# Kernel optimization log

Measured on AMD Instinct MI355X. Metric: run time of the kernel, lower is better.

Reference implementation:

```python
import jax, jax.numpy as jnp
import numpy as np

B, T, J, C = 64, 243, 17, 128   # batch, frames (temporal nodes), joints, channels
K = 4                            # neighbour_num for top-k similarity adjacency
EPS_LN = 1e-5
EPS_BN = 1e-5
S_GCN2ATTN = 0.5                 # fixed (requires_grad=False) scale; dropout is identity in eval


def setup_inputs() -> dict:
    key = jax.random.key(0)
    ks = jax.random.split(key, 4)
    s = np.sqrt(2.0 / C).astype(np.float32)  # GCN weight init scale
    return {
        "x": jax.random.normal(ks[0], (B, T, J, C), jnp.float32),
        "attention_feat": jax.random.normal(ks[1], (B, T, J, C), jnp.float32),
        "ln_w": jnp.ones((C,), jnp.float32),
        "ln_b": jnp.zeros((C,), jnp.float32),
        "Uw": jax.random.normal(ks[2], (C, C), jnp.float32) * s,
        "Ub": jnp.zeros((C,), jnp.float32),
        "Vw": jax.random.normal(ks[3], (C, C), jnp.float32) * s,
        "Vb": jnp.zeros((C,), jnp.float32),
        "bn_w": jnp.ones((T,), jnp.float32),   # BatchNorm1d(num_nodes=T), eval mode
        "bn_b": jnp.zeros((T,), jnp.float32),
        "ls1": jnp.full((C,), 1e-5, jnp.float32),  # layer_scale_1
    }


def reference(x, attention_feat, ln_w, ln_b, Uw, Ub, Vw, Vb, bn_w, bn_b, ls1):
    res = x
    # norm1: LayerNorm over channel dim
    mu = jnp.mean(x, axis=-1, keepdims=True)
    var = jnp.mean(jnp.square(x - mu), axis=-1, keepdims=True)
    xn = (x - mu) * jax.lax.rsqrt(var + EPS_LN) * ln_w + ln_b

    # temporal GCN: (B, T, J, C) -> (B*J, T, C)
    y = jnp.transpose(xn, (0, 2, 1, 3)).reshape(B * J, T, C)

    # dynamic adjacency via top-k similarity
    sim = jnp.einsum('ntc,nsc->nts', y, y)                 # [B*J, T, T]
    thr = jax.lax.top_k(sim, K)[0][..., -1:]               # k-th largest per row
    adj = (sim >= thr).astype(y.dtype)

    # D^{-1/2} A D^{-1/2} (degrees detached in original)
    dinv = jax.lax.stop_gradient(jnp.sum(adj, axis=-1)) ** -0.5  # [B*J, T]
    norm_adj = dinv[:, :, None] * adj * dinv[:, None, :]

    agg = jnp.einsum('nts,nsc->ntc', norm_adj, y @ Vw.T + Vb)
    h = agg + y @ Uw.T + Ub
    # eval-mode BatchNorm1d over T channel (running_mean=0, running_var=1)
    h = h * (bn_w * jax.lax.rsqrt(jnp.asarray(1.0 + EPS_BN, h.dtype)))[None, :, None] + bn_b[None, :, None]
    z = jax.nn.relu(y + h)                                 # dim_in == dim_out residual

    gcn_out = jnp.transpose(z.reshape(B, J, T, C), (0, 2, 1, 3))  # back to [B, T, J, C]

    gx = ls1 * gcn_out                                     # layer_scale_1 (drop_path = identity)
    graph_feat = gx * S_GCN2ATTN                           # gcn2Attn dropout identity in eval
    out = gx + attention_feat + res
    return out, graph_feat
```

## Files before the change

kernel.cpp:

```cpp
#include <hip/hip_runtime.h>

#define B_ 64
#define T_ 243
#define J_ 17
#define C_ 128
#define JC (J_*C_)
#define NTOT (B_*T_*J_*C_)

#define YOFF    0
#define YVOFF   34816
#define NBROFF  69632
#define BNWOFF  70656
#define BNBOFF  71680
#define UBOFF   72704
#define LSOFF   73216
#define SMEM_BYTES 73728
#define YSTR 136

typedef float f32x4 __attribute__((ext_vector_type(4)));
typedef float f32x2 __attribute__((ext_vector_type(2)));

__device__ __forceinline__ unsigned pkf8(float a, float b, float c, float d){
  int p = __builtin_amdgcn_cvt_pk_fp8_f32(a, b, 0, false);
  p = __builtin_amdgcn_cvt_pk_fp8_f32(c, d, p, true);
  return (unsigned)p;
}

template<int CTRL>
__device__ __forceinline__ float dppadd(float v){
  int t = __builtin_amdgcn_update_dpp(0, __float_as_int(v), CTRL, 0xf, 0xf, true);
  return v + __int_as_float(t);
}
__device__ __forceinline__ float swz16(float v){
  return __int_as_float(__builtin_amdgcn_ds_swizzle(__float_as_int(v), 0x401F));
}

#define PINS(x, a0,a1,a2,a3) do { \
  float t_ = fmaxf(a0,(x)), m_ = fminf(a0,(x)); a0 = t_; \
  float t2_ = fmaxf(a1,m_); m_ = fminf(a1,m_); a1 = t2_; \
  float t3_ = fmaxf(a2,m_); m_ = fminf(a2,m_); a2 = t3_; \
  a3 = fmaxf(a3,m_); \
} while(0)
#define MM(p,q) do { float h_=fmaxf(p,q); q=fminf(p,q); p=h_; } while(0)

extern "C" __global__ void __launch_bounds__(1024, 8)
graphblock_kernel(const float* __restrict__ x, const float* __restrict__ att,
                  const float* __restrict__ lnw, const float* __restrict__ lnb,
                  const float* __restrict__ Uw, const float* __restrict__ Ubv,
                  const float* __restrict__ Vw, const float* __restrict__ Vbv,
                  const float* __restrict__ bnw, const float* __restrict__ bnb,
                  const float* __restrict__ ls1, float* __restrict__ out)
{
  extern __shared__ char smem[];
  const int tid = threadIdx.x;
  const int w = tid >> 6, l = tid & 63;
  const int lr = l & 15, lg = l >> 4;
  const int n = blockIdx.x, b = n / J_, j = n % J_;
  const long nbase = (long)b*T_*JC + (long)j*C_;
  const int cs = w & 7, rh = w >> 3;
  const int ch0 = cs*16 + lg*4;

  if (tid < 256) {
    bool v = tid < T_;
    ((float*)(smem+BNWOFF))[tid] = v ? bnw[tid]*rsqrtf(1.0f+1e-5f) : 0.f;
    ((float*)(smem+BNBOFF))[tid] = v ? bnb[tid] : 0.f;
  } else if (tid < 384) {
    int c = tid - 256;
    ((float*)(smem+UBOFF))[c] = Ubv[c];
    ((float*)(smem+LSOFF))[c] = ls1[c];
  }

  {
    const int lh = l >> 5, lc = l & 31;
    const float4 lw4 = *(const float4*)(lnw + lc*4);
    const float4 lb4 = *(const float4*)(lnb + lc*4);
    float4 p[8];
    #pragma unroll
    for (int i=0;i<8;i++){
      const int r = i*32 + w*2 + lh;
      p[i] = make_float4(0.f,0.f,0.f,0.f);
      if (r < T_) p[i] = *(const float4*)(x + nbase + (long)r*JC + lc*4);
    }
    #pragma unroll
    for (int i=0;i<8;i++){
      const int r = i*32 + w*2 + lh;
      unsigned pk = 0u;
      if (r < T_) {
        float4 v = p[i];
        float s = (v.x+v.y)+(v.z+v.w);
        float q = (v.x*v.x+v.y*v.y)+(v.z*v.z+v.w*v.w);
        s = dppadd<0xB1>(s);  q = dppadd<0xB1>(q);
        s = dppadd<0x4E>(s);  q = dppadd<0x4E>(q);
        s = dppadd<0x124>(s); q = dppadd<0x124>(q);
        s = dppadd<0x128>(s); q = dppadd<0x128>(q);
        s += swz16(s);        q += swz16(q);
        float mu = s*(1.f/128.f);
        float rs = rsqrtf(q*(1.f/128.f)-mu*mu+1e-5f);
        pk = pkf8((v.x-mu)*rs*lw4.x+lb4.x, (v.y-mu)*rs*lw4.y+lb4.y,
                  (v.z-mu)*rs*lw4.z+lb4.z, (v.w-mu)*rs*lw4.w+lb4.w);
      }
      *(unsigned*)(smem + YOFF + r*YSTR + lc*4) = pk;
    }
  }
  __syncthreads();

  {
    const int tcol = w*16 + lr;
    long bfr[4];
    #pragma unroll
    for (int kk=0;kk<4;kk++)
      bfr[kk] = *(const long*)(smem + YOFF + tcol*YSTR + kk*32 + lg*8);
    float v0=-3e38f, v1=-3e38f, v2=-3e38f, v3=-3e38f;
    #pragma unroll 4
    for (int st=0; st<16; st++){
      f32x4 acc = {0.f,0.f,0.f,0.f};
      #pragma unroll
      for (int kk=0;kk<4;kk++){
        long afr = *(const long*)(smem + YOFF + (st*16+lr)*YSTR + kk*32 + lg*8);
        acc = __builtin_amdgcn_mfma_f32_16x16x32_fp8_fp8(afr, bfr[kk], acc, 0,0,0);
      }
      #pragma unroll
      for (int reg=0;reg<4;reg++){
        const int sidx = st*16 + lg*4 + reg;
        unsigned u = (__float_as_uint(acc[reg]) & 0xffffff00u) | (unsigned)(sidx & 0xff);
        float pv = (sidx < T_) ? __uint_as_float(u) : -3e38f;
        PINS(pv, v0,v1,v2,v3);
      }
    }
    #pragma unroll
    for (int m=16;m<64;m<<=1){
      float c0=__shfl_xor(v0,m,64), c1=__shfl_xor(v1,m,64),
            c2=__shfl_xor(v2,m,64), c3=__shfl_xor(v3,m,64);
      float d0=fmaxf(v0,c3), d1=fmaxf(v1,c2), d2=fmaxf(v2,c1), d3=fmaxf(v3,c0);
      MM(d0,d1); MM(d2,d3); MM(d0,d2); MM(d1,d3); MM(d1,d2);
      v0=d0; v1=d1; v2=d2; v3=d3;
    }
    if (lg==0){
      unsigned pk = (__float_as_uint(v0) & 0xffu)
                  | ((__float_as_uint(v1) & 0xffu) << 8)
                  | ((__float_as_uint(v2) & 0xffu) << 16)
                  | ((__float_as_uint(v3) & 0xffu) << 24);
      *(unsigned*)(smem + NBROFF + tcol*4) = pk;
    }
  }

  long ufr[4], vfr[4];
  {
    const int crw = cs*16 + lr;
    #pragma unroll
    for (int kk=0;kk<4;kk++){
      const float4* pu = (const float4*)(Uw + crw*C_ + kk*32 + lg*8);
      float4 a = pu[0], c = pu[1];
      union { long v; unsigned u[2]; } r;
      r.u[0] = pkf8(a.x,a.y,a.z,a.w); r.u[1] = pkf8(c.x,c.y,c.z,c.w);
      ufr[kk] = r.v;
      const float4* pv = (const float4*)(Vw + crw*C_ + kk*32 + lg*8);
      a = pv[0]; c = pv[1];
      r.u[0] = pkf8(a.x,a.y,a.z,a.w); r.u[1] = pkf8(c.x,c.y,c.z,c.w);
      vfr[kk] = r.v;
    }
  }
  const float4 vb4 = *(const float4*)(Vbv + ch0);

  #pragma unroll 2
  for (int tt=0; tt<8; tt++){
    const int t = (rh*8+tt)*16 + lr;
    f32x4 accV = {0.f,0.f,0.f,0.f};
    #pragma unroll
    for (int kk=0;kk<4;kk++){
      long yf = *(const long*)(smem + YOFF + t*YSTR + kk*32 + lg*8);
      accV = __builtin_amdgcn_mfma_f32_16x16x32_fp8_fp8(vfr[kk], yf, accV, 0,0,0);
    }
    *(unsigned*)(smem + YVOFF + t*YSTR + ch0) =
        pkf8(0.25f*(accV[0]+vb4.x), 0.25f*(accV[1]+vb4.y),
             0.25f*(accV[2]+vb4.z), 0.25f*(accV[3]+vb4.w));
  }
  __syncthreads();

  const float4 ub4 = *(const float4*)((const float*)(smem+UBOFF) + ch0);
  const float4 ls4 = *(const float4*)((const float*)(smem+LSOFF) + ch0);

  int   t_n  = (rh*8)*16 + lr;
  bool  ok_n = t_n < T_;
  long  g_n  = nbase + (long)t_n*JC + ch0;
  float4 px = make_float4(0,0,0,0), pa = make_float4(0,0,0,0);
  if (ok_n){ px = *(const float4*)(x+g_n); pa = *(const float4*)(att+g_n); }

  #pragma unroll
  for (int tt=0; tt<8; tt++){
    const int   t  = t_n;
    const bool  ok = ok_n;
    const long  g  = g_n;
    const float4 x4 = px, a4 = pa;
    if (tt < 7){
      t_n  = (rh*8+tt+1)*16 + lr;
      ok_n = t_n < T_;
      g_n  = nbase + (long)t_n*JC + ch0;
      px = make_float4(0,0,0,0); pa = make_float4(0,0,0,0);
      if (ok_n){ px = *(const float4*)(x+g_n); pa = *(const float4*)(att+g_n); }
    }
    f32x4 accU = {0.f,0.f,0.f,0.f};
    #pragma unroll
    for (int kk=0;kk<4;kk++){
      long yf = *(const long*)(smem + YOFF + t*YSTR + kk*32 + lg*8);
      accU = __builtin_amdgcn_mfma_f32_16x16x32_fp8_fp8(ufr[kk], yf, accU, 0,0,0);
    }
    unsigned nb = *(const unsigned*)(smem + NBROFF + t*4);
    const int s0 = (int)(nb & 0xffu), s1 = (int)((nb>>8)&0xffu),
              s2 = (int)((nb>>16)&0xffu), s3 = (int)((nb>>24)&0xffu);
    float ag0=0,ag1=0,ag2=0,ag3=0;
    {
      unsigned q; f32x2 e, o2;
      q = *(const unsigned*)(smem+YVOFF + s0*YSTR + ch0);
      e = __builtin_amdgcn_cvt_pk_f32_fp8(q,false); o2 = __builtin_amdgcn_cvt_pk_f32_fp8(q,true);
      ag0+=e[0]; ag1+=e[1]; ag2+=o2[0]; ag3+=o2[1];
      q = *(const unsigned*)(smem+YVOFF + s1*YSTR + ch0);
      e = __builtin_amdgcn_cvt_pk_f32_fp8(q,false); o2 = __builtin_amdgcn_cvt_pk_f32_fp8(q,true);
      ag0+=e[0]; ag1+=e[1]; ag2+=o2[0]; ag3+=o2[1];
      q = *(const unsigned*)(smem+YVOFF + s2*YSTR + ch0);
      e = __builtin_amdgcn_cvt_pk_f32_fp8(q,false); o2 = __builtin_amdgcn_cvt_pk_f32_fp8(q,true);
      ag0+=e[0]; ag1+=e[1]; ag2+=o2[0]; ag3+=o2[1];
      q = *(const unsigned*)(smem+YVOFF + s3*YSTR + ch0);
      e = __builtin_amdgcn_cvt_pk_f32_fp8(q,false); o2 = __builtin_amdgcn_cvt_pk_f32_fp8(q,true);
      ag0+=e[0]; ag1+=e[1]; ag2+=o2[0]; ag3+=o2[1];
    }
    float yo0,yo1,yo2,yo3;
    {
      unsigned q = *(const unsigned*)(smem + YOFF + t*YSTR + ch0);
      f32x2 e = __builtin_amdgcn_cvt_pk_f32_fp8(q,false);
      f32x2 o2 = __builtin_amdgcn_cvt_pk_f32_fp8(q,true);
      yo0=e[0]; yo1=e[1]; yo2=o2[0]; yo3=o2[1];
    }
    const float bw = ((const float*)(smem+BNWOFF))[t];
    const float bb = ((const float*)(smem+BNBOFF))[t];
    f32x4 o, gf;
    {
      float h = (accU[0] + ag0 + ub4.x)*bw + bb;
      float gx = ls4.x * fmaxf(0.f, yo0 + h);
      o[0] = gx + a4.x + x4.x; gf[0] = gx*0.5f;
    }{
      float h = (accU[1] + ag1 + ub4.y)*bw + bb;
      float gx = ls4.y * fmaxf(0.f, yo1 + h);
      o[1] = gx + a4.y + x4.y; gf[1] = gx*0.5f;
    }{
      float h = (accU[2] + ag2 + ub4.z)*bw + bb;
      float gx = ls4.z * fmaxf(0.f, yo2 + h);
      o[2] = gx + a4.z + x4.z; gf[2] = gx*0.5f;
    }{
      float h = (accU[3] + ag3 + ub4.w)*bw + bb;
      float gx = ls4.w * fmaxf(0.f, yo3 + h);
      o[3] = gx + a4.w + x4.w; gf[3] = gx*0.5f;
    }
    if (ok){
      *(f32x4*)(out+g)      = o;
      *(f32x4*)(out+NTOT+g) = gf;
    }
  }
}

extern "C" void kernel_launch(void* const* d_in, const int* in_sizes, int n_in,
                              void* d_out, int out_size, void* d_ws, size_t ws_size,
                              hipStream_t stream) {
  hipFuncSetAttribute(reinterpret_cast<const void*>(graphblock_kernel),
                      hipFuncAttributeMaxDynamicSharedMemorySize, SMEM_BYTES);
  dim3 grid(B_ * J_);
  dim3 block(1024);
  graphblock_kernel<<<grid, block, SMEM_BYTES, stream>>>(
      (const float*)d_in[0],
      (const float*)d_in[1],
      (const float*)d_in[2],
      (const float*)d_in[3],
      (const float*)d_in[4],
      (const float*)d_in[5],
      (const float*)d_in[6],
      (const float*)d_in[7],
      (const float*)d_in[8],
      (const float*)d_in[9],
      (const float*)d_in[10],
      (float*)d_out);
}
```

Measured before the change: 194.7 us.

## Use persistent 1024-block grid with second pass for leftover graph nodes

Launches 1024 blocks instead of 1088, so the first 64 blocks each process two (b,j) graph nodes in a loop, separated by a barrier. The LayerNorm load phase is split into two halves of four rows to reduce live registers, and the V-projection loop is fully unrolled. This is meant to avoid a partial second wave of blocks, but those 64 blocks now run twice as long, which can create a tail of the same length.

Result: slower. 380.0 us (+95.2%).

```diff
diff --git a/kernel.cpp b/kernel.cpp
--- a/kernel.cpp
+++ b/kernel.cpp
@@ -6,6 +6,7 @@
 #define C_ 128
 #define JC (J_*C_)
 #define NTOT (B_*T_*J_*C_)
+#define NBLK 1088
 
 #define YOFF    0
 #define YVOFF   34816
@@ -55,8 +56,6 @@
   const int tid = threadIdx.x;
   const int w = tid >> 6, l = tid & 63;
   const int lr = l & 15, lg = l >> 4;
-  const int n = blockIdx.x, b = n / J_, j = n % J_;
-  const long nbase = (long)b*T_*JC + (long)j*C_;
   const int cs = w & 7, rh = w >> 3;
   const int ch0 = cs*16 + lg*4;
 
@@ -70,191 +69,205 @@
     ((float*)(smem+LSOFF))[c] = ls1[c];
   }
 
-  {
-    const int lh = l >> 5, lc = l & 31;
-    const float4 lw4 = *(const float4*)(lnw + lc*4);
-    const float4 lb4 = *(const float4*)(lnb + lc*4);
-    float4 p[8];
+  const int k = blockIdx.x;
+  const int niter = (k < (NBLK - 1024)) ? 2 : 1;
+
+  for (int it = 0; it < niter; ++it) {
+    const int n = k + it*1024;
+    const int b = n / J_, j = n % J_;
+    const long nbase = (long)b*T_*JC + (long)j*C_;
+
+    {
+      const int lh = l >> 5, lc = l & 31;
+      const float4 lw4 = *(const float4*)(lnw + lc*4);
+      const float4 lb4 = *(const float4*)(lnb + lc*4);
+      #pragma unroll
+      for (int half=0; half<2; half++){
+        float4 p[4];
+        #pragma unroll
+        for (int q2=0;q2<4;q2++){
+          const int r = (half*4+q2)*32 + w*2 + lh;
+          p[q2] = make_float4(0.f,0.f,0.f,0.f);
+          if (r < T_) p[q2] = *(const float4*)(x + nbase + (long)r*JC + lc*4);
+        }
+        #pragma unroll
+        for (int q2=0;q2<4;q2++){
+          const int r = (half*4+q2)*32 + w*2 + lh;
+          unsigned pk = 0u;
+          if (r < T_) {
+            float4 v = p[q2];
+            float s = (v.x+v.y)+(v.z+v.w);
+            float q = (v.x*v.x+v.y*v.y)+(v.z*v.z+v.w*v.w);
+            s = dppadd<0xB1>(s);  q = dppadd<0xB1>(q);
+            s = dppadd<0x4E>(s);  q = dppadd<0x4E>(q);
+            s = dppadd<0x124>(s); q = dppadd<0x124>(q);
+            s = dppadd<0x128>(s); q = dppadd<0x128>(q);
+            s += swz16(s);        q += swz16(q);
+            float mu = s*(1.f/128.f);
+            float rs = rsqrtf(q*(1.f/128.f)-mu*mu+1e-5f);
+            pk = pkf8((v.x-mu)*rs*lw4.x+lb4.x, (v.y-mu)*rs*lw4.y+lb4.y,
+                      (v.z-mu)*rs*lw4.z+lb4.z, (v.w-mu)*rs*lw4.w+lb4.w);
+          }
+          *(unsigned*)(smem + YOFF + r*YSTR + lc*4) = pk;
+        }
+      }
+    }
+    __syncthreads();
+
+    {
+      const int tcol = w*16 + lr;
+      long bfr[4];
+      #pragma unroll
+      for (int kk=0;kk<4;kk++)
+        bfr[kk] = *(const long*)(smem + YOFF + tcol*YSTR + kk*32 + lg*8);
+      float v0=-3e38f, v1=-3e38f, v2=-3e38f, v3=-3e38f;
+      #pragma unroll 4
+      for (int st=0; st<16; st++){
+        f32x4 acc = {0.f,0.f,0.f,0.f};
+        #pragma unroll
+        for (int kk=0;kk<4;kk++){
+          long afr = *(const long*)(smem + YOFF + (st*16+lr)*YSTR + kk*32 + lg*8);
+          acc = __builtin_amdgcn_mfma_f32_16x16x32_fp8_fp8(afr, bfr[kk], acc, 0,0,0);
+        }
+        #pragma unroll
+        for (int reg=0;reg<4;reg++){
+          const int sidx = st*16 + lg*4 + reg;
+          unsigned uu = (__float_as_uint(acc[reg]) & 0xffffff00u) | (unsigned)(sidx & 0xff);
+          float pv = (sidx < T_) ? __uint_as_float(uu) : -3e38f;
+          PINS(pv, v0,v1,v2,v3);
+        }
+      }
+      #pragma unroll
+      for (int m=16;m<64;m<<=1){
+        float c0=__shfl_xor(v0,m,64), c1=__shfl_xor(v1,m,64),
+              c2=__shfl_xor(v2,m,64), c3=__shfl_xor(v3,m,64);
+        float d0=fmaxf(v0,c3), d1=fmaxf(v1,c2), d2=fmaxf(v2,c1), d3=fmaxf(v3,c0);
+        MM(d0,d1); MM(d2,d3); MM(d0,d2); MM(d1,d3); MM(d1,d2);
+        v0=d0; v1=d1; v2=d2; v3=d3;
+      }
+      if (lg==0){
+        unsigned pk = (__float_as_uint(v0) & 0xffu)
+                    | ((__float_as_uint(v1) & 0xffu) << 8)
+                    | ((__float_as_uint(v2) & 0xffu) << 16)
+                    | ((__float_as_uint(v3) & 0xffu) << 24);
+        *(unsigned*)(smem + NBROFF + tcol*4) = pk;
+      }
+    }
+
+    long ufr[4], vfr[4];
+    {
+      const int crw = cs*16 + lr;
+      #pragma unroll
+      for (int kk=0;kk<4;kk++){
+        const float4* pu = (const float4*)(Uw + crw*C_ + kk*32 + lg*8);
+        float4 a = pu[0], c = pu[1];
+        union { long v; unsigned u[2]; } r;
+        r.u[0] = pkf8(a.x,a.y,a.z,a.w); r.u[1] = pkf8(c.x,c.y,c.z,c.w);
+        ufr[kk] = r.v;
+        const float4* pv = (const float4*)(Vw + crw*C_ + kk*32 + lg*8);
+        a = pv[0]; c = pv[1];
+        r.u[0] = pkf8(a.x,a.y,a.z,a.w); r.u[1] = pkf8(c.x,c.y,c.z,c.w);
+        vfr[kk] = r.v;
+      }
+    }
+    const float4 vb4 = *(const float4*)(Vbv + ch0);
+
+    int   t_n  = (rh*8)*16 + lr;
+    bool  ok_n = t_n < T_;
+    long  g_n  = nbase + (long)t_n*JC + ch0;
+    float4 px = make_float4(0,0,0,0), pa = make_float4(0,0,0,0);
+    if (ok_n){ px = *(const float4*)(x+g_n); pa = *(const float4*)(att+g_n); }
+
     #pragma unroll
-    for (int i=0;i<8;i++){
-      const int r = i*32 + w*2 + lh;
-      p[i] = make_float4(0.f,0.f,0.f,0.f);
-      if (r < T_) p[i] = *(const float4*)(x + nbase + (long)r*JC + lc*4);
-    }
+    for (int tt=0; tt<8; tt++){
+      const int t = (rh*8+tt)*16 + lr;
+      f32x4 accV = {0.f,0.f,0.f,0.f};
+      #pragma unroll
+      for (int kk=0;kk<4;kk++){
+        long yf = *(const long*)(smem + YOFF + t*YSTR + kk*32 + lg*8);
+        accV = __builtin_amdgcn_mfma_f32_16x16x32_fp8_fp8(vfr[kk], yf, accV, 0,0,0);
+      }
+      *(unsigned*)(smem + YVOFF + t*YSTR + ch0) =
+          pkf8(0.25f*(accV[0]+vb4.x), 0.25f*(accV[1]+vb4.y),
+               0.25f*(accV[2]+vb4.z), 0.25f*(accV[3]+vb4.w));
+    }
+    __syncthreads();
+
+    const float4 ub4 = *(const float4*)((const float*)(smem+UBOFF) + ch0);
+    const float4 ls4 = *(const float4*)((const float*)(smem+LSOFF) + ch0);
+
     #pragma unroll
-    for (int i=0;i<8;i++){
-      const int r = i*32 + w*2 + lh;
-      unsigned pk = 0u;
-      if (r < T_) {
-        float4 v = p[i];
-        float s = (v.x+v.y)+(v.z+v.w);
-        float q = (v.x*v.x+v.y*v.y)+(v.z*v.z+v.w*v.w);
-        s = dppadd<0xB1>(s);  q = dppadd<0xB1>(q);
-        s = dppadd<0x4E>(s);  q = dppadd<0x4E>(q);
-        s = dppadd<0x124>(s); q = dppadd<0x124>(q);
-        s = dppadd<0x128>(s); q = dppadd<0x128>(q);
-        s += swz16(s);        q += swz16(q);
-        float mu = s*(1.f/128.f);
-        float rs = rsqrtf(q*(1.f/128.f)-mu*mu+1e-5f);
-        pk = pkf8((v.x-mu)*rs*lw4.x+lb4.x, (v.y-mu)*rs*lw4.y+lb4.y,
-                  (v.z-mu)*rs*lw4.z+lb4.z, (v.w-mu)*rs*lw4.w+lb4.w);
-      }
-      *(unsigned*)(smem + YOFF + r*YSTR + lc*4) = pk;
-    }
-  }
-  __syncthreads();
-
-  {
-    const int tcol = w*16 + lr;
-    long bfr[4];
-    #pragma unroll
-    for (int kk=0;kk<4;kk++)
-      bfr[kk] = *(const long*)(smem + YOFF + tcol*YSTR + kk*32 + lg*8);
-    float v0=-3e38f, v1=-3e38f, v2=-3e38f, v3=-3e38f;
-    #pragma unroll 4
-    for (int st=0; st<16; st++){
-      f32x4 acc = {0.f,0.f,0.f,0.f};
+    for (int tt=0; tt<8; tt++){
+      const int   t  = t_n;
+      const bool  ok = ok_n;
+      const long  g  = g_n;
+      const float4 x4 = px, a4 = pa;
+      if (tt < 7){
+        t_n  = (rh*8+tt+1)*16 + lr;
+        ok_n = t_n < T_;
+        g_n  = nbase + (long)t_n*JC + ch0;
+        px = make_float4(0,0,0,0); pa = make_float4(0,0,0,0);
+        if (ok_n){ px = *(const float4*)(x+g_n); pa = *(const float4*)(att+g_n); }
+      }
+      f32x4 accU = {0.f,0.f,0.f,0.f};
       #pragma unroll
       for (int kk=0;kk<4;kk++){
-        long afr = *(const long*)(smem + YOFF + (st*16+lr)*YSTR + kk*32 + lg*8);
-        acc = __builtin_amdgcn_mfma_f32_16x16x32_fp8_fp8(afr, bfr[kk], acc, 0,0,0);
-      }
-      #pragma unroll
-      for (int reg=0;reg<4;reg++){
-        const int sidx = st*16 + lg*4 + reg;
-        unsigned u = (__float_as_uint(acc[reg]) & 0xffffff00u) | (unsigned)(sidx & 0xff);
-        float pv = (sidx < T_) ? __uint_as_float(u) : -3e38f;
-        PINS(pv, v0,v1,v2,v3);
-      }
-    }
-    #pragma unroll
-    for (int m=16;m<64;m<<=1){
-      float c0=__shfl_xor(v0,m,64), c1=__shfl_xor(v1,m,64),
-            c2=__shfl_xor(v2,m,64), c3=__shfl_xor(v3,m,64);
-      float d0=fmaxf(v0,c3), d1=fmaxf(v1,c2), d2=fmaxf(v2,c1), d3=fmaxf(v3,c0);
-      MM(d0,d1); MM(d2,d3); MM(d0,d2); MM(d1,d3); MM(d1,d2);
-      v0=d0; v1=d1; v2=d2; v3=d3;
-    }
-    if (lg==0){
-      unsigned pk = (__float_as_uint(v0) & 0xffu)
-                  | ((__float_as_uint(v1) & 0xffu) << 8)
-                  | ((__float_as_uint(v2) & 0xffu) << 16)
-                  | ((__float_as_uint(v3) & 0xffu) << 24);
-      *(unsigned*)(smem + NBROFF + tcol*4) = pk;
-    }
-  }
-
-  long ufr[4], vfr[4];
-  {
-    const int crw = cs*16 + lr;
-    #pragma unroll
-    for (int kk=0;kk<4;kk++){
-      const float4* pu = (const float4*)(Uw + crw*C_ + kk*32 + lg*8);
-      float4 a = pu[0], c = pu[1];
-      union { long v; unsigned u[2]; } r;
-      r.u[0] = pkf8(a.x,a.y,a.z,a.w); r.u[1] = pkf8(c.x,c.y,c.z,c.w);
-      ufr[kk] = r.v;
-      const float4* pv = (const float4*)(Vw + crw*C_ + kk*32 + lg*8);
-      a = pv[0]; c = pv[1];
-      r.u[0] = pkf8(a.x,a.y,a.z,a.w); r.u[1] = pkf8(c.x,c.y,c.z,c.w);
-      vfr[kk] = r.v;
-    }
-  }
-  const float4 vb4 = *(const float4*)(Vbv + ch0);
-
-  #pragma unroll 2
-  for (int tt=0; tt<8; tt++){
-    const int t = (rh*8+tt)*16 + lr;
-    f32x4 accV = {0.f,0.f,0.f,0.f};
-    #pragma unroll
-    for (int kk=0;kk<4;kk++){
-      long yf = *(const long*)(smem + YOFF + t*YSTR + kk*32 + lg*8);
-      accV = __builtin_amdgcn_mfma_f32_16x16x32_fp8_fp8(vfr[kk], yf, accV, 0,0,0);
-    }
-    *(unsigned*)(smem + YVOFF + t*YSTR + ch0) =
-        pkf8(0.25f*(accV[0]+vb4.x), 0.25f*(accV[1]+vb4.y),
-             0.25f*(accV[2]+vb4.z), 0.25f*(accV[3]+vb4.w));
-  }
-  __syncthreads();
-
-  const float4 ub4 = *(const float4*)((const float*)(smem+UBOFF) + ch0);
-  const float4 ls4 = *(const float4*)((const float*)(smem+LSOFF) + ch0);
-
-  int   t_n  = (rh*8)*16 + lr;
-  bool  ok_n = t_n < T_;
-  long  g_n  = nbase + (long)t_n*JC + ch0;
-  float4 px = make_float4(0,0,0,0), pa = make_float4(0,0,0,0);
-  if (ok_n){ px = *(const float4*)(x+g_n); pa = *(const float4*)(att+g_n); }
-
-  #pragma unroll
-  for (int tt=0; tt<8; tt++){
-    const int   t  = t_n;
-    const bool  ok = ok_n;
-    const long  g  = g_n;
-    const float4 x4 = px, a4 = pa;
-    if (tt < 7){
-      t_n  = (rh*8+tt+1)*16 + lr;
-      ok_n = t_n < T_;
-      g_n  = nbase + (long)t_n*JC + ch0;
-      px = make_float4(0,0,0,0); pa = make_float4(0,0,0,0);
-      if (ok_n){ px = *(const float4*)(x+g_n); pa = *(const float4*)(att+g_n); }
-    }
-    f32x4 accU = {0.f,0.f,0.f,0.f};
-    #pragma unroll
-    for (int kk=0;kk<4;kk++){
-      long yf = *(const long*)(smem + YOFF + t*YSTR + kk*32 + lg*8);
-      accU = __builtin_amdgcn_mfma_f32_16x16x32_fp8_fp8(ufr[kk], yf, accU, 0,0,0);
-    }
-    unsigned nb = *(const unsigned*)(smem + NBROFF + t*4);
-    const int s0 = (int)(nb & 0xffu), s1 = (int)((nb>>8)&0xffu),
-              s2 = (int)((nb>>16)&0xffu), s3 = (int)((nb>>24)&0xffu);
-    float ag0=0,ag1=0,ag2=0,ag3=0;
-    {
-      unsigned q; f32x2 e, o2;
-      q = *(const unsigned*)(smem+YVOFF + s0*YSTR + ch0);
-      e = __builtin_amdgcn_cvt_pk_f32_fp8(q,false); o2 = __builtin_amdgcn_cvt_pk_f32_fp8(q,true);
-      ag0+=e[0]; ag1+=e[1]; ag2+=o2[0]; ag3+=o2[1];
-      q = *(const unsigned*)(smem+YVOFF + s1*YSTR + ch0);
-      e = __builtin_amdgcn_cvt_pk_f32_fp8(q,false); o2 = __builtin_amdgcn_cvt_pk_f32_fp8(q,true);
-      ag0+=e[0]; ag1+=e[1]; ag2+=o2[0]; ag3+=o2[1];
-      q = *(const unsigned*)(smem+YVOFF + s2*YSTR + ch0);
-      e = __builtin_amdgcn_cvt_pk_f32_fp8(q,false); o2 = __builtin_amdgcn_cvt_pk_f32_fp8(q,true);
-      ag0+=e[0]; ag1+=e[1]; ag2+=o2[0]; ag3+=o2[1];
-      q = *(const unsigned*)(smem+YVOFF + s3*YSTR + ch0);
-      e = __builtin_amdgcn_cvt_pk_f32_fp8(q,false); o2 = __builtin_amdgcn_cvt_pk_f32_fp8(q,true);
-      ag0+=e[0]; ag1+=e[1]; ag2+=o2[0]; ag3+=o2[1];
-    }
-    float yo0,yo1,yo2,yo3;
-    {
-      unsigned q = *(const unsigned*)(smem + YOFF + t*YSTR + ch0);
-      f32x2 e = __builtin_amdgcn_cvt_pk_f32_fp8(q,false);
-      f32x2 o2 = __builtin_amdgcn_cvt_pk_f32_fp8(q,true);
-      yo0=e[0]; yo1=e[1]; yo2=o2[0]; yo3=o2[1];
-    }
-    const float bw = ((const float*)(smem+BNWOFF))[t];
-    const float bb = ((const float*)(smem+BNBOFF))[t];
-    f32x4 o, gf;
-    {
-      float h = (accU[0] + ag0 + ub4.x)*bw + bb;
-      float gx = ls4.x * fmaxf(0.f, yo0 + h);
-      o[0] = gx + a4.x + x4.x; gf[0] = gx*0.5f;
-    }{
-      float h = (accU[1] + ag1 + ub4.y)*bw + bb;
-      float gx = ls4.y * fmaxf(0.f, yo1 + h);
-      o[1] = gx + a4.y + x4.y; gf[1] = gx*0.5f;
-    }{
-      float h = (accU[2] + ag2 + ub4.z)*bw + bb;
-      float gx = ls4.z * fmaxf(0.f, yo2 + h);
-      o[2] = gx + a4.z + x4.z; gf[2] = gx*0.5f;
-    }{
-      float h = (accU[3] + ag3 + ub4.w)*bw + bb;
-      float gx = ls4.w * fmaxf(0.f, yo3 + h);
-      o[3] = gx + a4.w + x4.w; gf[3] = gx*0.5f;
-    }
-    if (ok){
-      *(f32x4*)(out+g)      = o;
-      *(f32x4*)(out+NTOT+g) = gf;
-    }
+        long yf = *(const long*)(smem + YOFF + t*YSTR + kk*32 + lg*8);
+        accU = __builtin_amdgcn_mfma_f32_16x16x32_fp8_fp8(ufr[kk], yf, accU, 0,0,0);
+      }
+      unsigned nb = *(const unsigned*)(smem + NBROFF + t*4);
+      const int s0 = (int)(nb & 0xffu), s1 = (int)((nb>>8)&0xffu),
+                s2 = (int)((nb>>16)&0xffu), s3 = (int)((nb>>24)&0xffu);
+      float ag0=0,ag1=0,ag2=0,ag3=0;
+      {
+        unsigned q; f32x2 e, o2;
+        q = *(const unsigned*)(smem+YVOFF + s0*YSTR + ch0);
+        e = __builtin_amdgcn_cvt_pk_f32_fp8(q,false); o2 = __builtin_amdgcn_cvt_pk_f32_fp8(q,true);
+        ag0+=e[0]; ag1+=e[1]; ag2+=o2[0]; ag3+=o2[1];
+        q = *(const unsigned*)(smem+YVOFF + s1*YSTR + ch0);
+        e = __builtin_amdgcn_cvt_pk_f32_fp8(q,false); o2 = __builtin_amdgcn_cvt_pk_f32_fp8(q,true);
+        ag0+=e[0]; ag1+=e[1]; ag2+=o2[0]; ag3+=o2[1];
+        q = *(const unsigned*)(smem+YVOFF + s2*YSTR + ch0);
+        e = __builtin_amdgcn_cvt_pk_f32_fp8(q,false); o2 = __builtin_amdgcn_cvt_pk_f32_fp8(q,true);
+        ag0+=e[0]; ag1+=e[1]; ag2+=o2[0]; ag3+=o2[1];
+        q = *(const unsigned*)(smem+YVOFF + s3*YSTR + ch0);
+        e = __builtin_amdgcn_cvt_pk_f32_fp8(q,false); o2 = __builtin_amdgcn_cvt_pk_f32_fp8(q,true);
+        ag0+=e[0]; ag1+=e[1]; ag2+=o2[0]; ag3+=o2[1];
+      }
+      float yo0,yo1,yo2,yo3;
+      {
+        unsigned q = *(const unsigned*)(smem + YOFF + t*YSTR + ch0);
+        f32x2 e = __builtin_amdgcn_cvt_pk_f32_fp8(q,false);
+        f32x2 o2 = __builtin_amdgcn_cvt_pk_f32_fp8(q,true);
+        yo0=e[0]; yo1=e[1]; yo2=o2[0]; yo3=o2[1];
+      }
+      const float bw = ((const float*)(smem+BNWOFF))[t];
+      const float bb = ((const float*)(smem+BNBOFF))[t];
+      f32x4 o, gf;
+      {
+        float h = (accU[0] + ag0 + ub4.x)*bw + bb;
+        float gx = ls4.x * fmaxf(0.f, yo0 + h);
+        o[0] = gx + a4.x + x4.x; gf[0] = gx*0.5f;
+      }{
+        float h = (accU[1] + ag1 + ub4.y)*bw + bb;
+        float gx = ls4.y * fmaxf(0.f, yo1 + h);
+        o[1] = gx + a4.y + x4.y; gf[1] = gx*0.5f;
+      }{
+        float h = (accU[2] + ag2 + ub4.z)*bw + bb;
+        float gx = ls4.z * fmaxf(0.f, yo2 + h);
+        o[2] = gx + a4.z + x4.z; gf[2] = gx*0.5f;
+      }{
+        float h = (accU[3] + ag3 + ub4.w)*bw + bb;
+        float gx = ls4.w * fmaxf(0.f, yo3 + h);
+        o[3] = gx + a4.w + x4.w; gf[3] = gx*0.5f;
+      }
+      if (ok){
+        *(f32x4*)(out+g)      = o;
+        *(f32x4*)(out+NTOT+g) = gf;
+      }
+    }
+
+    if (it+1 < niter) __syncthreads();
   }
 }
 
@@ -263,7 +276,7 @@
                               hipStream_t stream) {
   hipFuncSetAttribute(reinterpret_cast<const void*>(graphblock_kernel),
                       hipFuncAttributeMaxDynamicSharedMemorySize, SMEM_BYTES);
-  dim3 grid(B_ * J_);
+  dim3 grid(1024);
   dim3 block(1024);
   graphblock_kernel<<<grid, block, SMEM_BYTES, stream>>>(
       (const float*)d_in[0],
```

## Fold V projection into neighbor gather via MFMA and halve block size

Applied to the files above, without the earlier changes.

Drops the precomputed Y·V table in shared memory. Each output tile now runs four extra MFMAs that apply V to the four gathered neighbour rows of Y, and the V and U biases are merged into one per-channel vector. This shrinks LDS from about 72KB to 38KB, and the block drops from 1024 to 512 threads, with each wave covering all 16 time tiles for its channel slice. The intent is more resident blocks per CU and one fewer barrier-separated phase. The cost is four times the V-MFMA work, since V is applied per neighbour instead of once per row.

After: 303.7 us. +56.0%, slower.

```diff
diff --git a/kernel.cpp b/kernel.cpp
--- a/kernel.cpp
+++ b/kernel.cpp
@@ -8,13 +8,12 @@
 #define NTOT (B_*T_*J_*C_)
 
 #define YOFF    0
-#define YVOFF   34816
-#define NBROFF  69632
-#define BNWOFF  70656
-#define BNBOFF  71680
-#define UBOFF   72704
-#define LSOFF   73216
-#define SMEM_BYTES 73728
+#define NBROFF  34816
+#define BNWOFF  35840
+#define BNBOFF  36864
+#define BIASOFF 37888
+#define LSOFF   38400
+#define SMEM_BYTES 38912
 #define YSTR 136
 
 typedef float f32x4 __attribute__((ext_vector_type(4)));
@@ -43,7 +42,7 @@
 } while(0)
 #define MM(p,q) do { float h_=fmaxf(p,q); q=fminf(p,q); p=h_; } while(0)
 
-extern "C" __global__ void __launch_bounds__(1024, 8)
+extern "C" __global__ void __launch_bounds__(512, 8)
 graphblock_kernel(const float* __restrict__ x, const float* __restrict__ att,
                   const float* __restrict__ lnw, const float* __restrict__ lnb,
                   const float* __restrict__ Uw, const float* __restrict__ Ubv,
@@ -57,8 +56,7 @@
   const int lr = l & 15, lg = l >> 4;
   const int n = blockIdx.x, b = n / J_, j = n % J_;
   const long nbase = (long)b*T_*JC + (long)j*C_;
-  const int cs = w & 7, rh = w >> 3;
-  const int ch0 = cs*16 + lg*4;
+  const int ch0 = w*16 + lg*4;
 
   if (tid < 256) {
     bool v = tid < T_;
@@ -66,46 +64,50 @@
     ((float*)(smem+BNBOFF))[tid] = v ? bnb[tid] : 0.f;
   } else if (tid < 384) {
     int c = tid - 256;
-    ((float*)(smem+UBOFF))[c] = Ubv[c];
-    ((float*)(smem+LSOFF))[c] = ls1[c];
+    ((float*)(smem+BIASOFF))[c] = Ubv[c] + Vbv[c];
+    ((float*)(smem+LSOFF))[c]   = ls1[c];
   }
 
   {
     const int lh = l >> 5, lc = l & 31;
     const float4 lw4 = *(const float4*)(lnw + lc*4);
     const float4 lb4 = *(const float4*)(lnb + lc*4);
-    float4 p[8];
-    #pragma unroll
-    for (int i=0;i<8;i++){
-      const int r = i*32 + w*2 + lh;
-      p[i] = make_float4(0.f,0.f,0.f,0.f);
-      if (r < T_) p[i] = *(const float4*)(x + nbase + (long)r*JC + lc*4);
-    }
-    #pragma unroll
-    for (int i=0;i<8;i++){
-      const int r = i*32 + w*2 + lh;
-      unsigned pk = 0u;
-      if (r < T_) {
-        float4 v = p[i];
-        float s = (v.x+v.y)+(v.z+v.w);
-        float q = (v.x*v.x+v.y*v.y)+(v.z*v.z+v.w*v.w);
-        s = dppadd<0xB1>(s);  q = dppadd<0xB1>(q);
-        s = dppadd<0x4E>(s);  q = dppadd<0x4E>(q);
-        s = dppadd<0x124>(s); q = dppadd<0x124>(q);
-        s = dppadd<0x128>(s); q = dppadd<0x128>(q);
-        s += swz16(s);        q += swz16(q);
-        float mu = s*(1.f/128.f);
-        float rs = rsqrtf(q*(1.f/128.f)-mu*mu+1e-5f);
-        pk = pkf8((v.x-mu)*rs*lw4.x+lb4.x, (v.y-mu)*rs*lw4.y+lb4.y,
-                  (v.z-mu)*rs*lw4.z+lb4.z, (v.w-mu)*rs*lw4.w+lb4.w);
-      }
-      *(unsigned*)(smem + YOFF + r*YSTR + lc*4) = pk;
+    #pragma unroll
+    for (int g2=0; g2<2; g2++){
+      float4 p[8];
+      #pragma unroll
+      for (int i=0;i<8;i++){
+        const int r = (g2*8+i)*16 + w*2 + lh;
+        p[i] = make_float4(0.f,0.f,0.f,0.f);
+        if (r < T_) p[i] = *(const float4*)(x + nbase + (long)r*JC + lc*4);
+      }
+      #pragma unroll
+      for (int i=0;i<8;i++){
+        const int r = (g2*8+i)*16 + w*2 + lh;
+        unsigned pk = 0u;
+        if (r < T_) {
+          float4 v = p[i];
+          float s = (v.x+v.y)+(v.z+v.w);
+          float q = (v.x*v.x+v.y*v.y)+(v.z*v.z+v.w*v.w);
+          s = dppadd<0xB1>(s);  q = dppadd<0xB1>(q);
+          s = dppadd<0x4E>(s);  q = dppadd<0x4E>(q);
+          s = dppadd<0x124>(s); q = dppadd<0x124>(q);
+          s = dppadd<0x128>(s); q = dppadd<0x128>(q);
+          s += swz16(s);        q += swz16(q);
+          float mu = s*(1.f/128.f);
+          float rs = rsqrtf(q*(1.f/128.f)-mu*mu+1e-5f);
+          pk = pkf8((v.x-mu)*rs*lw4.x+lb4.x, (v.y-mu)*rs*lw4.y+lb4.y,
+                    (v.z-mu)*rs*lw4.z+lb4.z, (v.w-mu)*rs*lw4.w+lb4.w);
+        }
+        *(unsigned*)(smem + YOFF + r*YSTR + lc*4) = pk;
+      }
     }
   }
   __syncthreads();
 
-  {
-    const int tcol = w*16 + lr;
+  #pragma unroll
+  for (int half=0; half<2; half++){
+    const int tcol = half*128 + w*16 + lr;
     long bfr[4];
     #pragma unroll
     for (int kk=0;kk<4;kk++)
@@ -122,8 +124,8 @@
       #pragma unroll
       for (int reg=0;reg<4;reg++){
         const int sidx = st*16 + lg*4 + reg;
-        unsigned u = (__float_as_uint(acc[reg]) & 0xffffff00u) | (unsigned)(sidx & 0xff);
-        float pv = (sidx < T_) ? __uint_as_float(u) : -3e38f;
+        unsigned uu = (__float_as_uint(acc[reg]) & 0xffffff00u) | (unsigned)(sidx & 0xff);
+        float pv = (sidx < T_) ? __uint_as_float(uu) : -3e38f;
         PINS(pv, v0,v1,v2,v3);
       }
     }
@@ -146,7 +148,7 @@
 
   long ufr[4], vfr[4];
   {
-    const int crw = cs*16 + lr;
+    const int crw = w*16 + lr;
     #pragma unroll
     for (int kk=0;kk<4;kk++){
       const float4* pu = (const float4*)(Uw + crw*C_ + kk*32 + lg*8);
@@ -156,73 +158,48 @@
       ufr[kk] = r.v;
       const float4* pv = (const float4*)(Vw + crw*C_ + kk*32 + lg*8);
       a = pv[0]; c = pv[1];
-      r.u[0] = pkf8(a.x,a.y,a.z,a.w); r.u[1] = pkf8(c.x,c.y,c.z,c.w);
+      r.u[0] = pkf8(0.25f*a.x,0.25f*a.y,0.25f*a.z,0.25f*a.w);
+      r.u[1] = pkf8(0.25f*c.x,0.25f*c.y,0.25f*c.z,0.25f*c.w);
       vfr[kk] = r.v;
     }
   }
-  const float4 vb4 = *(const float4*)(Vbv + ch0);
-
-  #pragma unroll 2
-  for (int tt=0; tt<8; tt++){
-    const int t = (rh*8+tt)*16 + lr;
-    f32x4 accV = {0.f,0.f,0.f,0.f};
-    #pragma unroll
-    for (int kk=0;kk<4;kk++){
-      long yf = *(const long*)(smem + YOFF + t*YSTR + kk*32 + lg*8);
-      accV = __builtin_amdgcn_mfma_f32_16x16x32_fp8_fp8(vfr[kk], yf, accV, 0,0,0);
-    }
-    *(unsigned*)(smem + YVOFF + t*YSTR + ch0) =
-        pkf8(0.25f*(accV[0]+vb4.x), 0.25f*(accV[1]+vb4.y),
-             0.25f*(accV[2]+vb4.z), 0.25f*(accV[3]+vb4.w));
-  }
   __syncthreads();
 
-  const float4 ub4 = *(const float4*)((const float*)(smem+UBOFF) + ch0);
-  const float4 ls4 = *(const float4*)((const float*)(smem+LSOFF) + ch0);
-
-  int   t_n  = (rh*8)*16 + lr;
-  bool  ok_n = t_n < T_;
+  int   t_n  = lr;
+  bool  ok_n = true;
   long  g_n  = nbase + (long)t_n*JC + ch0;
-  float4 px = make_float4(0,0,0,0), pa = make_float4(0,0,0,0);
-  if (ok_n){ px = *(const float4*)(x+g_n); pa = *(const float4*)(att+g_n); }
+  float4 px = *(const float4*)(x+g_n), pa = *(const float4*)(att+g_n);
 
   #pragma unroll
-  for (int tt=0; tt<8; tt++){
+  for (int tile=0; tile<16; tile++){
     const int   t  = t_n;
     const bool  ok = ok_n;
     const long  g  = g_n;
     const float4 x4 = px, a4 = pa;
-    if (tt < 7){
-      t_n  = (rh*8+tt+1)*16 + lr;
+    if (tile < 15){
+      t_n  = (tile+1)*16 + lr;
       ok_n = t_n < T_;
       g_n  = nbase + (long)t_n*JC + ch0;
       px = make_float4(0,0,0,0); pa = make_float4(0,0,0,0);
       if (ok_n){ px = *(const float4*)(x+g_n); pa = *(const float4*)(att+g_n); }
     }
-    f32x4 accU = {0.f,0.f,0.f,0.f};
-    #pragma unroll
-    for (int kk=0;kk<4;kk++){
-      long yf = *(const long*)(smem + YOFF + t*YSTR + kk*32 + lg*8);
-      accU = __builtin_amdgcn_mfma_f32_16x16x32_fp8_fp8(ufr[kk], yf, accU, 0,0,0);
-    }
-    unsigned nb = *(const unsigned*)(smem + NBROFF + t*4);
+    const unsigned nb = *(const unsigned*)(smem + NBROFF + t*4);
     const int s0 = (int)(nb & 0xffu), s1 = (int)((nb>>8)&0xffu),
               s2 = (int)((nb>>16)&0xffu), s3 = (int)((nb>>24)&0xffu);
-    float ag0=0,ag1=0,ag2=0,ag3=0;
-    {
-      unsigned q; f32x2 e, o2;
-      q = *(const unsigned*)(smem+YVOFF + s0*YSTR + ch0);
-      e = __builtin_amdgcn_cvt_pk_f32_fp8(q,false); o2 = __builtin_amdgcn_cvt_pk_f32_fp8(q,true);
-      ag0+=e[0]; ag1+=e[1]; ag2+=o2[0]; ag3+=o2[1];
-      q = *(const unsigned*)(smem+YVOFF + s1*YSTR + ch0);
-      e = __builtin_amdgcn_cvt_pk_f32_fp8(q,false); o2 = __builtin_amdgcn_cvt_pk_f32_fp8(q,true);
-      ag0+=e[0]; ag1+=e[1]; ag2+=o2[0]; ag3+=o2[1];
-      q = *(const unsigned*)(smem+YVOFF + s2*YSTR + ch0);
-      e = __builtin_amdgcn_cvt_pk_f32_fp8(q,false); o2 = __builtin_amdgcn_cvt_pk_f32_fp8(q,true);
-      ag0+=e[0]; ag1+=e[1]; ag2+=o2[0]; ag3+=o2[1];
-      q = *(const unsigned*)(smem+YVOFF + s3*YSTR + ch0);
-      e = __builtin_amdgcn_cvt_pk_f32_fp8(q,false); o2 = __builtin_amdgcn_cvt_pk_f32_fp8(q,true);
-      ag0+=e[0]; ag1+=e[1]; ag2+=o2[0]; ag3+=o2[1];
+    f32x4 accU = {0.f,0.f,0.f,0.f}, accV = {0.f,0.f,0.f,0.f};
+    #pragma unroll
+    for (int kk=0;kk<4;kk++){
+      const int co = kk*32 + lg*8;
+      long yf = *(const long*)(smem + YOFF + t*YSTR + co);
+      accU = __builtin_amdgcn_mfma_f32_16x16x32_fp8_fp8(ufr[kk], yf, accU, 0,0,0);
+      long b0 = *(const long*)(smem + YOFF + s0*YSTR + co);
+      accV = __builtin_amdgcn_mfma_f32_16x16x32_fp8_fp8(vfr[kk], b0, accV, 0,0,0);
+      long b1 = *(const long*)(smem + YOFF + s1*YSTR + co);
+      accV = __builtin_amdgcn_mfma_f32_16x16x32_fp8_fp8(vfr[kk], b1, accV, 0,0,0);
+      long b2 = *(const long*)(smem + YOFF + s2*YSTR + co);
+      accV = __builtin_amdgcn_mfma_f32_16x16x32_fp8_fp8(vfr[kk], b2, accV, 0,0,0);
+      long b3 = *(const long*)(smem + YOFF + s3*YSTR + co);
+      accV = __builtin_amdgcn_mfma_f32_16x16x32_fp8_fp8(vfr[kk], b3, accV, 0,0,0);
     }
     float yo0,yo1,yo2,yo3;
     {
@@ -231,23 +208,25 @@
       f32x2 o2 = __builtin_amdgcn_cvt_pk_f32_fp8(q,true);
       yo0=e[0]; yo1=e[1]; yo2=o2[0]; yo3=o2[1];
     }
-    const float bw = ((const float*)(smem+BNWOFF))[t];
-    const float bb = ((const float*)(smem+BNBOFF))[t];
+    const float  bw = ((const float*)(smem+BNWOFF))[t];
+    const float  bb = ((const float*)(smem+BNBOFF))[t];
+    const float4 uv4 = *(const float4*)((const float*)(smem+BIASOFF) + ch0);
+    const float4 ls4 = *(const float4*)((const float*)(smem+LSOFF)   + ch0);
     f32x4 o, gf;
     {
-      float h = (accU[0] + ag0 + ub4.x)*bw + bb;
+      float h = (accU[0] + accV[0] + uv4.x)*bw + bb;
       float gx = ls4.x * fmaxf(0.f, yo0 + h);
       o[0] = gx + a4.x + x4.x; gf[0] = gx*0.5f;
     }{
-      float h = (accU[1] + ag1 + ub4.y)*bw + bb;
+      float h = (accU[1] + accV[1] + uv4.y)*bw + bb;
       float gx = ls4.y * fmaxf(0.f, yo1 + h);
       o[1] = gx + a4.y + x4.y; gf[1] = gx*0.5f;
     }{
-      float h = (accU[2] + ag2 + ub4.z)*bw + bb;
+      float h = (accU[2] + accV[2] + uv4.z)*bw + bb;
       float gx = ls4.z * fmaxf(0.f, yo2 + h);
       o[2] = gx + a4.z + x4.z; gf[2] = gx*0.5f;
     }{
-      float h = (accU[3] + ag3 + ub4.w)*bw + bb;
+      float h = (accU[3] + accV[3] + uv4.w)*bw + bb;
       float gx = ls4.w * fmaxf(0.f, yo3 + h);
       o[3] = gx + a4.w + x4.w; gf[3] = gx*0.5f;
     }
@@ -264,7 +243,7 @@
   hipFuncSetAttribute(reinterpret_cast<const void*>(graphblock_kernel),
                       hipFuncAttributeMaxDynamicSharedMemorySize, SMEM_BYTES);
   dim3 grid(B_ * J_);
-  dim3 block(1024);
+  dim3 block(512);
   graphblock_kernel<<<grid, block, SMEM_BYTES, stream>>>(
       (const float*)d_in[0],
       (const float*)d_in[1],
```

## Halve block size to 512 threads, doubling per-wave work in each phase

Applied to the files above, without the earlier changes.

Launches 512-thread blocks instead of 1024 and remaps every phase (LayerNorm load, similarity top-k, V projection, output epilogue) so each wave covers twice as many rows or columns. This cuts block-wide barrier cost and makes each wave handle all 16 column tiles of its channel slice. The trade-off is fewer waves per block to hide latency, but with 72KB of LDS per block, two blocks may fit per CU. Longer unrolled loops could raise register pressure.

Result: faster. 190.5 us (-2.2%).

```diff
diff --git a/kernel.cpp b/kernel.cpp
--- a/kernel.cpp
+++ b/kernel.cpp
@@ -43,7 +43,7 @@
 } while(0)
 #define MM(p,q) do { float h_=fmaxf(p,q); q=fminf(p,q); p=h_; } while(0)
 
-extern "C" __global__ void __launch_bounds__(1024, 8)
+extern "C" __global__ void __launch_bounds__(512, 4)
 graphblock_kernel(const float* __restrict__ x, const float* __restrict__ att,
                   const float* __restrict__ lnw, const float* __restrict__ lnb,
                   const float* __restrict__ Uw, const float* __restrict__ Ubv,
@@ -57,8 +57,7 @@
   const int lr = l & 15, lg = l >> 4;
   const int n = blockIdx.x, b = n / J_, j = n % J_;
   const long nbase = (long)b*T_*JC + (long)j*C_;
-  const int cs = w & 7, rh = w >> 3;
-  const int ch0 = cs*16 + lg*4;
+  const int ch0 = w*16 + lg*4;
 
   if (tid < 256) {
     bool v = tid < T_;
@@ -74,38 +73,42 @@
     const int lh = l >> 5, lc = l & 31;
     const float4 lw4 = *(const float4*)(lnw + lc*4);
     const float4 lb4 = *(const float4*)(lnb + lc*4);
-    float4 p[8];
-    #pragma unroll
-    for (int i=0;i<8;i++){
-      const int r = i*32 + w*2 + lh;
-      p[i] = make_float4(0.f,0.f,0.f,0.f);
-      if (r < T_) p[i] = *(const float4*)(x + nbase + (long)r*JC + lc*4);
-    }
-    #pragma unroll
-    for (int i=0;i<8;i++){
-      const int r = i*32 + w*2 + lh;
-      unsigned pk = 0u;
-      if (r < T_) {
-        float4 v = p[i];
-        float s = (v.x+v.y)+(v.z+v.w);
-        float q = (v.x*v.x+v.y*v.y)+(v.z*v.z+v.w*v.w);
-        s = dppadd<0xB1>(s);  q = dppadd<0xB1>(q);
-        s = dppadd<0x4E>(s);  q = dppadd<0x4E>(q);
-        s = dppadd<0x124>(s); q = dppadd<0x124>(q);
-        s = dppadd<0x128>(s); q = dppadd<0x128>(q);
-        s += swz16(s);        q += swz16(q);
-        float mu = s*(1.f/128.f);
-        float rs = rsqrtf(q*(1.f/128.f)-mu*mu+1e-5f);
-        pk = pkf8((v.x-mu)*rs*lw4.x+lb4.x, (v.y-mu)*rs*lw4.y+lb4.y,
-                  (v.z-mu)*rs*lw4.z+lb4.z, (v.w-mu)*rs*lw4.w+lb4.w);
-      }
-      *(unsigned*)(smem + YOFF + r*YSTR + lc*4) = pk;
+    #pragma unroll
+    for (int g2=0; g2<2; g2++){
+      float4 p[8];
+      #pragma unroll
+      for (int i=0;i<8;i++){
+        const int r = (g2*8+i)*16 + w*2 + lh;
+        p[i] = make_float4(0.f,0.f,0.f,0.f);
+        if (r < T_) p[i] = *(const float4*)(x + nbase + (long)r*JC + lc*4);
+      }
+      #pragma unroll
+      for (int i=0;i<8;i++){
+        const int r = (g2*8+i)*16 + w*2 + lh;
+        unsigned pk = 0u;
+        if (r < T_) {
+          float4 v = p[i];
+          float s = (v.x+v.y)+(v.z+v.w);
+          float q = (v.x*v.x+v.y*v.y)+(v.z*v.z+v.w*v.w);
+          s = dppadd<0xB1>(s);  q = dppadd<0xB1>(q);
+          s = dppadd<0x4E>(s);  q = dppadd<0x4E>(q);
+          s = dppadd<0x124>(s); q = dppadd<0x124>(q);
+          s = dppadd<0x128>(s); q = dppadd<0x128>(q);
+          s += swz16(s);        q += swz16(q);
+          float mu = s*(1.f/128.f);
+          float rs = rsqrtf(q*(1.f/128.f)-mu*mu+1e-5f);
+          pk = pkf8((v.x-mu)*rs*lw4.x+lb4.x, (v.y-mu)*rs*lw4.y+lb4.y,
+                    (v.z-mu)*rs*lw4.z+lb4.z, (v.w-mu)*rs*lw4.w+lb4.w);
+        }
+        *(unsigned*)(smem + YOFF + r*YSTR + lc*4) = pk;
+      }
     }
   }
   __syncthreads();
 
-  {
-    const int tcol = w*16 + lr;
+  #pragma unroll
+  for (int half=0; half<2; half++){
+    const int tcol = half*128 + w*16 + lr;
     long bfr[4];
     #pragma unroll
     for (int kk=0;kk<4;kk++)
@@ -122,8 +125,8 @@
       #pragma unroll
       for (int reg=0;reg<4;reg++){
         const int sidx = st*16 + lg*4 + reg;
-        unsigned u = (__float_as_uint(acc[reg]) & 0xffffff00u) | (unsigned)(sidx & 0xff);
-        float pv = (sidx < T_) ? __uint_as_float(u) : -3e38f;
+        unsigned uu = (__float_as_uint(acc[reg]) & 0xffffff00u) | (unsigned)(sidx & 0xff);
+        float pv = (sidx < T_) ? __uint_as_float(uu) : -3e38f;
         PINS(pv, v0,v1,v2,v3);
       }
     }
@@ -146,7 +149,7 @@
 
   long ufr[4], vfr[4];
   {
-    const int crw = cs*16 + lr;
+    const int crw = w*16 + lr;
     #pragma unroll
     for (int kk=0;kk<4;kk++){
       const float4* pu = (const float4*)(Uw + crw*C_ + kk*32 + lg*8);
@@ -162,9 +165,9 @@
   }
   const float4 vb4 = *(const float4*)(Vbv + ch0);
 
-  #pragma unroll 2
-  for (int tt=0; tt<8; tt++){
-    const int t = (rh*8+tt)*16 + lr;
+  #pragma unroll 4
+  for (int tt=0; tt<16; tt++){
+    const int t = tt*16 + lr;
     f32x4 accV = {0.f,0.f,0.f,0.f};
     #pragma unroll
     for (int kk=0;kk<4;kk++){
@@ -180,20 +183,19 @@
   const float4 ub4 = *(const float4*)((const float*)(smem+UBOFF) + ch0);
   const float4 ls4 = *(const float4*)((const float*)(smem+LSOFF) + ch0);
 
-  int   t_n  = (rh*8)*16 + lr;
-  bool  ok_n = t_n < T_;
+  int   t_n  = lr;
+  bool  ok_n = true;
   long  g_n  = nbase + (long)t_n*JC + ch0;
-  float4 px = make_float4(0,0,0,0), pa = make_float4(0,0,0,0);
-  if (ok_n){ px = *(const float4*)(x+g_n); pa = *(const float4*)(att+g_n); }
+  float4 px = *(const float4*)(x+g_n), pa = *(const float4*)(att+g_n);
 
   #pragma unroll
-  for (int tt=0; tt<8; tt++){
+  for (int tt=0; tt<16; tt++){
     const int   t  = t_n;
     const bool  ok = ok_n;
     const long  g  = g_n;
     const float4 x4 = px, a4 = pa;
-    if (tt < 7){
-      t_n  = (rh*8+tt+1)*16 + lr;
+    if (tt < 15){
+      t_n  = (tt+1)*16 + lr;
       ok_n = t_n < T_;
       g_n  = nbase + (long)t_n*JC + ch0;
       px = make_float4(0,0,0,0); pa = make_float4(0,0,0,0);
@@ -264,7 +266,7 @@
   hipFuncSetAttribute(reinterpret_cast<const void*>(graphblock_kernel),
                       hipFuncAttributeMaxDynamicSharedMemorySize, SMEM_BYTES);
   dim3 grid(B_ * J_);
-  dim3 block(1024);
+  dim3 block(512);
   graphblock_kernel<<<grid, block, SMEM_BYTES, stream>>>(
       (const float*)d_in[0],
       (const float*)d_in[1],
```
